# Kernel optimization log

Measured on AMD Instinct MI355X. Metric: run time of the kernel, lower is better.

Reference implementation:

```python
import jax, jax.numpy as jnp
import numpy as np
from jax import lax

# ---- fixed configuration (matches init_kwargs / input_specs) ----
L, E, V, F, HU, HL, S = 32, 1024, 2048, 8, 128, 2, 7
D0, D1R, D1E = 512, 129, 640
D = S + 1                      # path dimension = num_slices + 1
SIGLEN = D + D * D + D * D * D # iisignature.siglength(8, 3) = 584
FINAL = F * 2 * SIGLEN         # 9344
EPS = 1e-5                     # BatchNorm eps


def _bn(x, g, b):
    # BatchNorm1d in training mode: biased batch statistics over axis 0
    mu = x.mean(0)
    var = x.var(0)
    return (x - mu) / jnp.sqrt(var + EPS) * g + b


def _mlp(x, Win, bin_, gin, betain, Wh, bh, gh, betah, Wout, bout, gout, betaout):
    # eigf: Linear+BN+ReLU blocks, 1 -> HU -> ... -> HU -> 1
    h = jax.nn.relu(_bn(x @ Win.T + bin_, gin, betain))
    for l in range(HL):
        h = jax.nn.relu(_bn(h @ Wh[l].T + bh[l], gh[l], betah[l]))
    o = jax.nn.relu(_bn(h @ Wout.T + bout, gout, betaout))
    return o[:, 0]


# ---- path signature, level 3, via Chen's identity (replaces iisignature.sig) ----
def _seg(dx):
    s1 = dx
    s2 = jnp.outer(s1, dx).reshape(-1) * 0.5
    s3 = jnp.outer(s2, dx).reshape(-1) / 3.0
    return (s1, s2, s3)


def _chen(Sg, T):
    s1, s2, s3 = Sg
    t1, t2, t3 = T
    r1 = s1 + t1
    r2 = s2 + t2 + jnp.outer(s1, t1).reshape(-1)
    r3 = s3 + t3 + jnp.outer(s1, t2).reshape(-1) + jnp.outer(s2, t1).reshape(-1)
    return (r1, r2, r3)


def _sig3(path):  # path [P, D] -> [SIGLEN]
    dX = path[1:] - path[:-1]

    def step(Sg, dx):
        return _chen(Sg, _seg(dx)), None

    Sg, _ = lax.scan(step, _seg(dX[0]), dX[1:])
    return jnp.concatenate(Sg)


def _diagram_sig(vals, W_proj, b_proj):
    # Conv1d(1, S, kernel=2, stride=2) == pairwise projection; then sort, prepend time axis
    pairs = vals.reshape(-1, 2)                      # [P, 2]
    P = pairs.shape[0]
    proj = jnp.einsum('pk,sk->sp', pairs, W_proj[:, 0, :]) + b_proj[:, None]  # [S, P]
    proj = jnp.sort(proj, axis=-1)
    t = jnp.arange(P, dtype=vals.dtype) / (P * (P + 1) / 2.0)
    path = jnp.concatenate([t[None, :], proj], axis=0).T  # [P, D]
    return _sig3(path)


def setup_inputs() -> dict:
    key = jax.random.key(0)
    ks = iter(jax.random.split(key, 16))
    nrm = lambda kk, shp, sc: jax.random.normal(kk, shp, jnp.float32) * sc
    inp = {
        "eigenvalues": jax.random.uniform(next(ks), (L, E), jnp.float32),
        "eigenvectors_sq": jax.random.uniform(next(ks), (L, E, V), jnp.float32) / E,
        "dgm0": jax.random.randint(next(ks), (L, F, D0), 0, V, jnp.int32),
        "dgm1rel": jax.random.randint(next(ks), (L, F, D1R), 0, V, jnp.int32),
        "dgm1ext": jax.random.randint(next(ks), (L, F, D1E), 0, V, jnp.int32),
        "mlp_Win": nrm(next(ks), (F, HU, 1), 1.0),
        "mlp_bin": jnp.zeros((F, HU), jnp.float32),
        "mlp_gin": jnp.ones((F, HU), jnp.float32),
        "mlp_betain": jnp.zeros((F, HU), jnp.float32),
        "mlp_Wh": nrm(next(ks), (F, HL, HU, HU), 1.0 / np.sqrt(HU)),
        "mlp_bh": jnp.zeros((F, HL, HU), jnp.float32),
        "mlp_gh": jnp.ones((F, HL, HU), jnp.float32),
        "mlp_betah": jnp.zeros((F, HL, HU), jnp.float32),
        "mlp_Wout": nrm(next(ks), (F, 1, HU), 1.0 / np.sqrt(HU)),
        "mlp_bout": jnp.zeros((F, 1), jnp.float32),
        "mlp_gout": jnp.ones((F, 1), jnp.float32),
        "mlp_betaout": jnp.zeros((F, 1), jnp.float32),
        "W_proj": nrm(next(ks), (S, 1, 2), 0.7),
        "b_proj": jnp.zeros((S,), jnp.float32),
        "W_fin": nrm(next(ks), (1, FINAL), 1.0 / np.sqrt(FINAL)),
        "b_fin": jnp.zeros((1,), jnp.float32),
        "g_fin": jnp.ones((1,), jnp.float32),
        "beta_fin": jnp.zeros((1,), jnp.float32),
    }
    return inp


def reference(eigenvalues, eigenvectors_sq, dgm0, dgm1rel, dgm1ext,
              mlp_Win, mlp_bin, mlp_gin, mlp_betain,
              mlp_Wh, mlp_bh, mlp_gh, mlp_betah,
              mlp_Wout, mlp_bout, mlp_gout, mlp_betaout,
              W_proj, b_proj, W_fin, b_fin, g_fin, beta_fin):
    flat = eigenvalues.reshape(-1, 1)  # [L*E, 1], sample-major like the torch flatten
    evs = jax.vmap(lambda *p: _mlp(flat, *p))(
        mlp_Win, mlp_bin, mlp_gin, mlp_betain,
        mlp_Wh, mlp_bh, mlp_gh, mlp_betah,
        mlp_Wout, mlp_bout, mlp_gout, mlp_betaout)  # [F, L*E]
    # per-sample filtration values: evs_transformed[:, slice_i] @ eigvecsq_i
    f = jnp.einsum('fle,lev->lfv', evs.reshape(F, L, E), eigenvectors_sq)  # [L, F, V]
    fv = f.reshape(L * F, V)
    d0 = jnp.take_along_axis(fv, dgm0.reshape(L * F, D0), axis=1)
    rel = jnp.take_along_axis(fv, dgm1rel.reshape(L * F, D1R), axis=1)
    # torch.arange(len-1, 0, -1): reversed, dropping element 0
    Dgm0 = jnp.concatenate([d0, rel[:, 1:][:, ::-1]], axis=1)  # [L*F, 640]
    Dgm1 = jnp.take_along_axis(fv, dgm1ext.reshape(L * F, D1E), axis=1)
    sig0 = jax.vmap(lambda v: _diagram_sig(v, W_proj, b_proj))(Dgm0)  # [L*F, SIGLEN]
    sig1 = jax.vmap(lambda v: _diagram_sig(v, W_proj, b_proj))(Dgm1)
    x = jnp.concatenate([sig0, sig1], axis=-1).reshape(L, FINAL)
    out = x @ W_fin.T + b_fin  # dropout p=0.0 -> identity
    return _bn(out, g_fin, beta_fin)  # [L, 1]
```

## Files before the change

kernel.cpp:

```cpp
#include <hip/hip_runtime.h>
#include <cfloat>
#include <math.h>

#define N_SAMP 32768
#define FF 8
#define HU 128
#define EE 1024
#define VV 2048
#define PP 320
#define SIGLEN 584
#define FINAL_W 9344

typedef unsigned short u16;
typedef unsigned int u32;
typedef short s16x8 __attribute__((ext_vector_type(8)));
typedef float f32x4 __attribute__((ext_vector_type(4)));

__device__ __forceinline__ u16 f2bf(float v) {
  u32 u = __float_as_uint(v);
  return (u16)((u + 0x7fffu + ((u >> 16) & 1u)) >> 16);
}
__device__ __forceinline__ float bf2f(u16 h) {
  return __uint_as_float(((u32)h) << 16);
}
__device__ __forceinline__ void split3(float v, u16& h, u16& m, u16& l) {
  h = f2bf(v);
  float r = v - bf2f(h);
  m = f2bf(r);
  float r2 = r - bf2f(m);
  l = f2bf(r2);
}

__device__ __forceinline__ double wave_red(double v) {
#pragma unroll
  for (int off = 32; off > 0; off >>= 1) v += __shfl_xor(v, off, 64);
  return v;
}

#define WPAD_ROW 40
#define WPAD_CHUNK (128 * WPAD_ROW)
#define WPAD_LAYER (4 * WPAD_CHUNK)
#define WPAD_F (2 * WPAD_LAYER)
#define WPAD_TOTAL (FF * WPAD_F)

__global__ __launch_bounds__(256) void k_prep(const float* __restrict__ W,
                                              u16* __restrict__ Hh, u16* __restrict__ Hm,
                                              u16* __restrict__ Hl,
                                              const float* __restrict__ x,
                                              double* __restrict__ D) {
  __shared__ double r1[4], r2[4];
  const int bid = blockIdx.x, tid = threadIdx.x;
  if (bid < 1024) {
    int i = bid * 256 + tid;
    u16 h, m, l;
    split3(W[i], h, m, l);
    int k = i & 127, n = (i >> 7) & 127, f2l = i >> 14;
    int out = f2l * WPAD_LAYER + (k >> 5) * WPAD_CHUNK + n * WPAD_ROW + (k & 31);
    Hh[out] = h; Hm[out] = m; Hl[out] = l;
  } else if (bid < 1056) {
    int b = bid - 1024;
    double s1 = 0.0, s2 = 0.0;
    int base = b * 1024 + tid;
#pragma unroll
    for (int r = 0; r < 4; ++r) {
      double v = (double)x[base + r * 256];
      s1 += v; s2 += v * v;
    }
    s1 = wave_red(s1); s2 = wave_red(s2);
    int wave = tid >> 6, lane = tid & 63;
    if (lane == 0) { r1[wave] = s1; r2[wave] = s2; }
    __syncthreads();
    if (tid == 0) {
      D[b * 2 + 0] = r1[0] + r1[1] + r1[2] + r1[3];
      D[b * 2 + 1] = r2[0] + r2[1] + r2[2] + r2[3];
    }
  } else {
    int q = (bid - 1056) * 256 + tid;
    if (q < 4145) D[64 + q] = 0.0;
  }
}

template<int MODE>
__global__ __launch_bounds__(256, 2)
void k_mgemm(const float* __restrict__ Ain,
             const double* __restrict__ xp,
             const float* __restrict__ w_in,
             const float* __restrict__ g_in,
             const float* __restrict__ beta_in,
             const double* __restrict__ stats_in,
             const float* __restrict__ gM1,
             const float* __restrict__ betaM1,
             const u16* __restrict__ Wh_,
             const u16* __restrict__ Wm_,
             const u16* __restrict__ Wl_,
             const float* __restrict__ bb, int bstride,
             float* __restrict__ Yt_out,
             double* __restrict__ stats) {
  __shared__ u16 SB[6][128 * 40];
  __shared__ float p0[HU], p1[HU], biasl[HU], xl[HU];
  u16* Ah = SB[0]; u16* Am = SB[1]; u16* Al = SB[2];
  u16* Bh = SB[3]; u16* Bm = SB[4]; u16* Bl = SB[5];

  const int tid = threadIdx.x;
  const int f = blockIdx.y;
  const int m0 = blockIdx.x * 128;
  const int lane = tid & 63, ln = tid & 15, quad = (tid >> 4) & 3, wave = tid >> 6;

  if (tid < HU) {
    biasl[tid] = bb[(size_t)f * bstride + tid];
    if (MODE == 0) {
      double S1 = 0.0, S2 = 0.0;
#pragma unroll
      for (int r = 0; r < 32; ++r) { S1 += xp[r * 2]; S2 += xp[r * 2 + 1]; }
      double mx = S1 * (1.0 / 32768.0);
      double vx = S2 * (1.0 / 32768.0) - mx * mx;
      if (vx < 0) vx = 0;
      float w = w_in[f * HU + tid];
      double inv = 1.0 / sqrt((double)w * (double)w * vx + 1e-5);
      float sj = (float)inv * g_in[f * HU + tid] * w;
      p0[tid] = sj;
      p1[tid] = beta_in[f * HU + tid] - (float)mx * sj;
      xl[tid] = Ain[m0 + tid];
    } else {
      int idx = f * HU + tid;
      double S1 = stats_in[idx * 2 + 0], S2 = stats_in[idx * 2 + 1];
      double mean = S1 * (1.0 / 32768.0);
      double var = S2 * (1.0 / 32768.0) - mean * mean;
      if (var < 0) var = 0;
      double inv = 1.0 / sqrt(var + 1e-5);
      float gg = gM1[f * 256 + tid];
      float scv = (float)inv * gg;
      p0[tid] = scv;
      p1[tid] = betaM1[f * 256 + tid] - (float)mean * scv;
    }
  }

  f32x4 acc[2][8];
#pragma unroll
  for (int mt = 0; mt < 2; ++mt)
#pragma unroll
    for (int u = 0; u < 8; ++u) acc[mt][u] = (f32x4){0.f, 0.f, 0.f, 0.f};

  __syncthreads();

  for (int kk = 0; kk < 128; kk += 32) {
    {
      const int chunk = kk >> 5;
      const u16* gH = Wh_ + (size_t)f * WPAD_F + chunk * WPAD_CHUNK;
      const u16* gM = Wm_ + (size_t)f * WPAD_F + chunk * WPAD_CHUNK;
      const u16* gL = Wl_ + (size_t)f * WPAD_F + chunk * WPAD_CHUNK;
#pragma unroll
      for (int t = 0; t < 8; ++t) {
        int flat = wave + t * 4;
        if (flat < 30) {
          int L = (flat >= 20) ? 2 : (flat >= 10 ? 1 : 0);
          int p = flat - L * 10;
          const u16* g = (L == 0 ? gH : (L == 1 ? gM : gL)) + p * 512 + lane * 8;
          u16* d = (L == 0 ? Bh : (L == 1 ? Bm : Bl)) + p * 512;
          __builtin_amdgcn_global_load_lds(
              (const __attribute__((address_space(1))) void*)g,
              (__attribute__((address_space(3))) void*)d, 16, 0, 0);
        }
      }
    }
    if (MODE == 0) {
      const int m = tid >> 1, kh = (tid & 1) * 16;
      const float xv = xl[m];
      u32 ph[8], pm[8], pl[8];
#pragma unroll
      for (int jp = 0; jp < 8; ++jp) {
        u16 h0, m_0, l0, h1, m_1, l1;
        int k = kh + jp * 2;
        split3(fmaxf(fmaf(xv, p0[kk + k], p1[kk + k]), 0.f), h0, m_0, l0);
        split3(fmaxf(fmaf(xv, p0[kk + k + 1], p1[kk + k + 1]), 0.f), h1, m_1, l1);
        ph[jp] = (u32)h0 | ((u32)h1 << 16);
        pm[jp] = (u32)m_0 | ((u32)m_1 << 16);
        pl[jp] = (u32)l0 | ((u32)l1 << 16);
      }
      int off = m * 40 + kh;
      *(uint4*)&Ah[off] = make_uint4(ph[0], ph[1], ph[2], ph[3]);
      *(uint4*)&Ah[off + 8] = make_uint4(ph[4], ph[5], ph[6], ph[7]);
      *(uint4*)&Am[off] = make_uint4(pm[0], pm[1], pm[2], pm[3]);
      *(uint4*)&Am[off + 8] = make_uint4(pm[4], pm[5], pm[6], pm[7]);
      *(uint4*)&Al[off] = make_uint4(pl[0], pl[1], pl[2], pl[3]);
      *(uint4*)&Al[off + 8] = make_uint4(pl[4], pl[5], pl[6], pl[7]);
    } else {
#pragma unroll
      for (int r = 0; r < 4; ++r) {
        int flat = tid + r * 256;
        int m = flat & 127, kq = flat >> 7;
        const float* src = Ain + ((size_t)(f * HU + kk + kq * 4)) * N_SAMP + m0 + m;
        u32 ph[2], pm[2], pl[2];
#pragma unroll
        for (int ip = 0; ip < 2; ++ip) {
          int k = kq * 4 + ip * 2;
          float v0 = fmaxf(fmaf(src[(size_t)(ip * 2) * N_SAMP], p0[kk + k], p1[kk + k]), 0.f);
          float v1 = fmaxf(fmaf(src[(size_t)(ip * 2 + 1) * N_SAMP], p0[kk + k + 1], p1[kk + k + 1]), 0.f);
          u16 h0, m_0, l0, h1, m_1, l1;
          split3(v0, h0, m_0, l0);
          split3(v1, h1, m_1, l1);
          ph[ip] = (u32)h0 | ((u32)h1 << 16);
          pm[ip] = (u32)m_0 | ((u32)m_1 << 16);
          pl[ip] = (u32)l0 | ((u32)l1 << 16);
        }
        int off = m * 40 + kq * 4;
        *(uint2*)&Ah[off] = make_uint2(ph[0], ph[1]);
        *(uint2*)&Am[off] = make_uint2(pm[0], pm[1]);
        *(uint2*)&Al[off] = make_uint2(pl[0], pl[1]);
      }
    }
    __syncthreads();
    s16x8 af0[3], af1[3];
    {
      int r0 = (wave * 32 + ln) * 40 + quad * 8;
      int r1 = (wave * 32 + 16 + ln) * 40 + quad * 8;
      af0[0] = *(const s16x8*)&Ah[r0]; af0[1] = *(const s16x8*)&Am[r0]; af0[2] = *(const s16x8*)&Al[r0];
      af1[0] = *(const s16x8*)&Ah[r1]; af1[1] = *(const s16x8*)&Am[r1]; af1[2] = *(const s16x8*)&Al[r1];
    }
#pragma unroll
    for (int u = 0; u < 8; ++u) {
      int bo = (u * 16 + ln) * 40 + quad * 8;
      s16x8 bh = *(const s16x8*)&Bh[bo];
      s16x8 bm = *(const s16x8*)&Bm[bo];
      s16x8 bl = *(const s16x8*)&Bl[bo];
      f32x4 a0 = acc[0][u], a1 = acc[1][u];
      a0 = __builtin_amdgcn_mfma_f32_16x16x32_bf16(af0[0], bh, a0, 0, 0, 0);
      a1 = __builtin_amdgcn_mfma_f32_16x16x32_bf16(af1[0], bh, a1, 0, 0, 0);
      a0 = __builtin_amdgcn_mfma_f32_16x16x32_bf16(af0[1], bh, a0, 0, 0, 0);
      a1 = __builtin_amdgcn_mfma_f32_16x16x32_bf16(af1[1], bh, a1, 0, 0, 0);
      a0 = __builtin_amdgcn_mfma_f32_16x16x32_bf16(af0[0], bm, a0, 0, 0, 0);
      a1 = __builtin_amdgcn_mfma_f32_16x16x32_bf16(af1[0], bm, a1, 0, 0, 0);
      a0 = __builtin_amdgcn_mfma_f32_16x16x32_bf16(af0[2], bh, a0, 0, 0, 0);
      a1 = __builtin_amdgcn_mfma_f32_16x16x32_bf16(af1[2], bh, a1, 0, 0, 0);
      a0 = __builtin_amdgcn_mfma_f32_16x16x32_bf16(af0[1], bm, a0, 0, 0, 0);
      a1 = __builtin_amdgcn_mfma_f32_16x16x32_bf16(af1[1], bm, a1, 0, 0, 0);
      a0 = __builtin_amdgcn_mfma_f32_16x16x32_bf16(af0[0], bl, a0, 0, 0, 0);
      a1 = __builtin_amdgcn_mfma_f32_16x16x32_bf16(af1[0], bl, a1, 0, 0, 0);
      acc[0][u] = a0; acc[1][u] = a1;
    }
    __syncthreads();
  }

  float cs1[8], cs2[8];
#pragma unroll
  for (int u = 0; u < 8; ++u) { cs1[u] = 0.f; cs2[u] = 0.f; }
#pragma unroll
  for (int u = 0; u < 8; ++u) {
    float b = biasl[u * 16 + ln];
#pragma unroll
    for (int mt = 0; mt < 2; ++mt) {
#pragma unroll
      for (int reg = 0; reg < 4; ++reg) {
        float v = acc[mt][u][reg] + b;
        acc[mt][u][reg] = v;
        cs1[u] += v;
        cs2[u] = fmaf(v, v, cs2[u]);
      }
      float4 st = make_float4(acc[mt][u][0], acc[mt][u][1], acc[mt][u][2], acc[mt][u][3]);
      *(float4*)&Yt_out[((size_t)(f * HU + u * 16 + ln)) * N_SAMP + m0 + wave * 32 + mt * 16 + quad * 4] = st;
    }
  }
  float* red1 = (float*)&SB[0][0];
  float* red2 = red1 + 2048;
  int wq = wave * 4 + quad;
#pragma unroll
  for (int u = 0; u < 8; ++u) {
    red1[wq * 128 + u * 16 + ln] = cs1[u];
    red2[wq * 128 + u * 16 + ln] = cs2[u];
  }
  __syncthreads();
  {
    int which = tid >> 7, n = tid & 127;
    const float* rp = which ? red2 : red1;
    float s = 0.f;
#pragma unroll
    for (int r = 0; r < 16; ++r) s += rp[r * 128 + n];
    atomicAdd(&stats[(f * HU + n) * 2 + which], (double)s);
  }
}

__global__ __launch_bounds__(256, 4) void k_outlayer(const float* __restrict__ Yt,
                                                     const double* __restrict__ stats2,
                                                     const float* __restrict__ gh,
                                                     const float* __restrict__ betah,
                                                     const float* __restrict__ Wout,
                                                     const float* __restrict__ bout,
                                                     float* __restrict__ evs_pre,
                                                     double* __restrict__ stats3) {
  __shared__ float wj[HU], scl[HU], shl[HU];
  const int tid = threadIdx.x;
  const int f = blockIdx.y;
  const int i = (blockIdx.x * 256 + tid) * 2;
  if (tid < HU) {
    wj[tid] = Wout[f * HU + tid];
    int idx = f * HU + tid;
    double S1 = stats2[idx * 2 + 0], S2 = stats2[idx * 2 + 1];
    double mean = S1 * (1.0 / 32768.0);
    double var = S2 * (1.0 / 32768.0) - mean * mean;
    if (var < 0) var = 0;
    double inv = 1.0 / sqrt(var + 1e-5);
    float gg = gh[128 + f * 256 + tid];
    float scv = (float)inv * gg;
    scl[tid] = scv;
    shl[tid] = betah[128 + f * 256 + tid] - (float)mean * scv;
  }
  __syncthreads();
  const float2* base2 = (const float2*)(Yt + (size_t)f * HU * N_SAMP + i);
  float a0 = 0.f, a1 = 0.f;
#pragma unroll
  for (int j = 0; j < HU; ++j) {
    float2 y = base2[(size_t)j * (N_SAMP / 2)];
    a0 = fmaf(fmaxf(fmaf(y.x, scl[j], shl[j]), 0.f), wj[j], a0);
    a1 = fmaf(fmaxf(fmaf(y.y, scl[j], shl[j]), 0.f), wj[j], a1);
  }
  float yo0 = a0 + bout[f];
  float yo1 = a1 + bout[f];
  *(float2*)&evs_pre[(size_t)f * N_SAMP + i] = make_float2(yo0, yo1);
  double v0 = (double)yo0, v1 = (double)yo1;
  double s1 = wave_red(v0 + v1), s2 = wave_red(v0 * v0 + v1 * v1);
  __shared__ double r1[4], r2[4];
  int wave = tid >> 6, lane = tid & 63;
  if (lane == 0) { r1[wave] = s1; r2[wave] = s2; }
  __syncthreads();
  if (tid == 0) atomicAdd(&stats3[f * 2 + 0], r1[0] + r1[1] + r1[2] + r1[3]);
  if (tid == 1) atomicAdd(&stats3[f * 2 + 1], r2[0] + r2[1] + r2[2] + r2[3]);
}

__global__ __launch_bounds__(256) void k_einsum(const float* __restrict__ evs_pre,
                                                const double* __restrict__ stats3,
                                                const float* __restrict__ gout,
                                                const float* __restrict__ betaout,
                                                const float* __restrict__ eig,
                                                float* __restrict__ fv) {
  __shared__ __align__(16) float ev[FF * EE];
  __shared__ float scl3[FF], shl3[FF];
  const int tid = threadIdx.x;
  const int l = blockIdx.y;
  const int v0 = blockIdx.x * 256;
  if (tid < FF) {
    double S1 = stats3[tid * 2 + 0], S2 = stats3[tid * 2 + 1];
    double mean = S1 * (1.0 / 32768.0);
    double var = S2 * (1.0 / 32768.0) - mean * mean;
    if (var < 0) var = 0;
    double inv = 1.0 / sqrt(var + 1e-5);
    float gg = gout[tid];
    float scv = (float)inv * gg;
    scl3[tid] = scv;
    shl3[tid] = betaout[tid] - (float)mean * scv;
  }
  __syncthreads();
#pragma unroll
  for (int r = 0; r < 8; ++r) {
    int flat = tid + r * 256;
    int fch = flat >> 8, e4 = (flat & 255) * 4;
    float4 y = *(const float4*)&evs_pre[(size_t)fch * N_SAMP + l * EE + e4];
    float sv = scl3[fch], hv = shl3[fch];
    float* evp = &ev[fch * EE + e4];
    evp[0] = fmaxf(fmaf(y.x, sv, hv), 0.f);
    evp[1] = fmaxf(fmaf(y.y, sv, hv), 0.f);
    evp[2] = fmaxf(fmaf(y.z, sv, hv), 0.f);
    evp[3] = fmaxf(fmaf(y.w, sv, hv), 0.f);
  }
  __syncthreads();
  const float* up = eig + (size_t)l * EE * VV + v0 + tid;
  float acc[8] = {0, 0, 0, 0, 0, 0, 0, 0};
  for (int e0 = 0; e0 < EE; e0 += 32) {
    float u[32];
#pragma unroll
    for (int t = 0; t < 32; ++t) u[t] = up[(size_t)(e0 + t) * VV];
#pragma unroll
    for (int t = 0; t < 32; ++t) {
#pragma unroll
      for (int f = 0; f < 8; ++f) acc[f] = fmaf(ev[f * EE + e0 + t], u[t], acc[f]);
    }
  }
#pragma unroll
  for (int f = 0; f < 8; ++f) fv[((size_t)(l * FF + f)) * VV + v0 + tid] = acc[f];
}

__global__ __launch_bounds__(256) void k_diagram(const float* __restrict__ fv,
                                                 const int* __restrict__ dgm0,
                                                 const int* __restrict__ dgm1rel,
                                                 const int* __restrict__ dgm1ext,
                                                 const float* __restrict__ Wp,
                                                 const float* __restrict__ bp,
                                                 const float* __restrict__ Wf,
                                                 const float* __restrict__ bf,
                                                 const float* __restrict__ gfin,
                                                 const float* __restrict__ betafin,
                                                 double* __restrict__ outpre,
                                                 unsigned int* __restrict__ cnt,
                                                 float* __restrict__ dout) {
  __shared__ float vals[640];
  __shared__ float ps[7 * 512];
  __shared__ float dXl[320][8];
  __shared__ double rr[4];
  __shared__ unsigned int lastFlag;
  const int tid = threadIdx.x;
  const int bid = blockIdx.x;
  const int row = bid >> 1;
  const int c = bid & 1;
  const float* fvr = fv + (size_t)row * VV;

  for (int k = tid; k < 640; k += 256) {
    int idx;
    if (c == 0) idx = (k < 512) ? dgm0[(size_t)row * 512 + k] : dgm1rel[(size_t)row * 129 + (640 - k)];
    else        idx = dgm1ext[(size_t)row * 640 + k];
    vals[k] = fvr[idx];
  }
  __syncthreads();
  for (int q = tid; q < 7 * 512; q += 256) {
    int s = q >> 9, p = q & 511;
    float pv = 3.402823466e+38f;
    if (p < PP) pv = fmaf(Wp[2 * s + 1], vals[2 * p + 1], fmaf(Wp[2 * s], vals[2 * p], bp[s]));
    ps[s * 512 + p] = pv;
  }
  for (int k = 2; k <= 512; k <<= 1) {
    for (int j = k >> 1; j > 0; j >>= 1) {
      __syncthreads();
      for (int q = tid; q < 1792; q += 256) {
        int s = q >> 8, ip = q & 255;
        int i = ((ip & ~(j - 1)) << 1) | (ip & (j - 1));
        int p2 = i | j;
        float a = ps[s * 512 + i], b = ps[s * 512 + p2];
        bool up = ((i & k) == 0);
        if ((a > b) == up) { ps[s * 512 + i] = b; ps[s * 512 + p2] = a; }
      }
    }
  }
  __syncthreads();
  for (int q = tid; q < 319 * 8; q += 256) {
    int p = q >> 3, d = q & 7;
    dXl[p][d] = (d == 0) ? (1.0f / 51360.0f)
                         : ps[(d - 1) * 512 + p + 1] - ps[(d - 1) * 512 + p];
  }
  __syncthreads();
  {
    const int a = tid >> 5, b = (tid >> 2) & 7, dp = tid & 3;
    float s1a = 0.f, s2r = 0.f, s3r0 = 0.f, s3r1 = 0.f;
    for (int p = 0; p < 319; ++p) {
      float dxa = dXl[p][a];
      float dxb = dXl[p][b];
      float2 dd = *(const float2*)&dXl[p][dp * 2];
      float coefA = fmaf(dxa, (1.f / 3.f), s1a);
      float w = fmaf(0.5f * dxb, coefA, s2r);
      s2r = fmaf(dxb, fmaf(0.5f, dxa, s1a), s2r);
      s3r0 = fmaf(w, dd.x, s3r0);
      s3r1 = fmaf(w, dd.y, s3r1);
      s1a += dxa;
    }
    const int l = row >> 3, ff = row & 7;
    const int base = ff * (2 * SIGLEN) + c * SIGLEN;
    double part = (double)s3r0 * (double)Wf[base + 72 + (a * 8 + b) * 8 + dp * 2]
                + (double)s3r1 * (double)Wf[base + 72 + (a * 8 + b) * 8 + dp * 2 + 1];
    if (dp == 0) part += (double)s2r * (double)Wf[base + 8 + a * 8 + b];
    if (b == 0 && dp == 0) part += (double)s1a * (double)Wf[base + a];
    part = wave_red(part);
    int wv = tid >> 6, lnn = tid & 63;
    if (lnn == 0) rr[wv] = part;
    __syncthreads();
    if (tid == 0) {
      atomicAdd(&outpre[l], rr[0] + rr[1] + rr[2] + rr[3]);
      __threadfence();
      unsigned int old = atomicAdd(cnt, 1u);
      lastFlag = (old == 511u) ? 1u : 0u;
    }
    __syncthreads();
    if (lastFlag && tid < 64) {
      __threadfence();
      double v = 0.0;
      if (tid < 32) v = ((volatile double*)outpre)[tid] + (double)bf[0];
      double s1 = wave_red(v);
      double s2 = wave_red(v * v);
      double mean = s1 * (1.0 / 32.0);
      double var = s2 * (1.0 / 32.0) - mean * mean;
      if (var < 0) var = 0;
      double inv = 1.0 / sqrt(var + 1e-5);
      if (tid < 32) dout[tid] = (float)((v - mean) * inv * (double)gfin[0] + (double)betafin[0]);
    }
  }
}

extern "C" void kernel_launch(void* const* d_in, const int* in_sizes, int n_in,
                              void* d_out, int out_size, void* d_ws, size_t ws_size,
                              hipStream_t stream) {
  const float* eig     = (const float*)d_in[0];
  const float* eigsq   = (const float*)d_in[1];
  const int*   dgm0    = (const int*)d_in[2];
  const int*   dgm1rel = (const int*)d_in[3];
  const int*   dgm1ext = (const int*)d_in[4];
  const float* Win     = (const float*)d_in[5];
  const float* gin     = (const float*)d_in[7];
  const float* betain  = (const float*)d_in[8];
  const float* Wh      = (const float*)d_in[9];
  const float* bh      = (const float*)d_in[10];
  const float* gh      = (const float*)d_in[11];
  const float* betah   = (const float*)d_in[12];
  const float* Wout    = (const float*)d_in[13];
  const float* bout    = (const float*)d_in[14];
  const float* gout    = (const float*)d_in[15];
  const float* betaout = (const float*)d_in[16];
  const float* Wp      = (const float*)d_in[17];
  const float* bp      = (const float*)d_in[18];
  const float* Wfin    = (const float*)d_in[19];
  const float* bfin    = (const float*)d_in[20];
  const float* gfin    = (const float*)d_in[21];
  const float* betafin = (const float*)d_in[22];

  char* ws = (char*)d_ws;
  float*  Yt      = (float*)(ws);
  float*  evs_pre = (float*)(ws + 134217728u);
  float*  fv      = (float*)(ws + 135266304u);
  double* D       = (double*)(ws + 138576384u);
  double* xp      = D;
  double* stats1  = D + 64;
  double* stats2  = D + 2112;
  double* stats3  = D + 4160;
  double* outpre  = D + 4176;
  unsigned int* cnt = (unsigned int*)(D + 4208);
  u16*    Whh     = (u16*)(ws + 138612736u);
  u16*    Whm     = Whh + WPAD_TOTAL;
  u16*    Whl     = Whm + WPAD_TOTAL;

  k_prep<<<1073, 256, 0, stream>>>(Wh, Whh, Whm, Whl, eig, D);
  k_mgemm<0><<<dim3(256, FF), 256, 0, stream>>>(eig, xp, Win, gin, betain,
                                                nullptr, nullptr, nullptr,
                                                Whh, Whm, Whl,
                                                bh, 256, Yt, stats1);
  k_mgemm<1><<<dim3(256, FF), 256, 0, stream>>>(Yt, nullptr, nullptr, nullptr, nullptr,
                                                stats1, gh, betah,
                                                Whh + WPAD_LAYER, Whm + WPAD_LAYER, Whl + WPAD_LAYER,
                                                bh + 128, 256, Yt, stats2);
  k_outlayer<<<dim3(64, FF), 256, 0, stream>>>(Yt, stats2, gh, betah, Wout, bout,
                                               evs_pre, stats3);
  k_einsum<<<dim3(8, 32), 256, 0, stream>>>(evs_pre, stats3, gout, betaout, eigsq, fv);
  k_diagram<<<512, 256, 0, stream>>>(fv, dgm0, dgm1rel, dgm1ext, Wp, bp,
                                     Wfin, bfin, gfin, betafin, outpre, cnt,
                                     (float*)d_out);
}
```

Baseline: 663.9 us.

## Recompute first hidden layer in-register to avoid writing and rereading its activations

The first GEMM pass now only computes BatchNorm statistics and no longer stores its 128x32768x8 activation tensor. A second fused kernel recomputes layer 0 from the scalar input, applies BN+ReLU to the accumulators in registers, splits them into bf16 parts in shared memory and runs the second hidden-layer GEMM directly. This removes a large global write and a strided global read of the intermediate, at the cost of running the first layer's three-way-split MFMA GEMM twice.

```diff
diff --git a/kernel.cpp b/kernel.cpp
--- a/kernel.cpp
+++ b/kernel.cpp
@@ -80,22 +80,17 @@
   }
 }
 
-template<int MODE>
 __global__ __launch_bounds__(256, 2)
-void k_mgemm(const float* __restrict__ Ain,
-             const double* __restrict__ xp,
-             const float* __restrict__ w_in,
-             const float* __restrict__ g_in,
-             const float* __restrict__ beta_in,
-             const double* __restrict__ stats_in,
-             const float* __restrict__ gM1,
-             const float* __restrict__ betaM1,
-             const u16* __restrict__ Wh_,
-             const u16* __restrict__ Wm_,
-             const u16* __restrict__ Wl_,
-             const float* __restrict__ bb, int bstride,
-             float* __restrict__ Yt_out,
-             double* __restrict__ stats) {
+void k_stats0(const float* __restrict__ x,
+              const double* __restrict__ xp,
+              const float* __restrict__ w_in,
+              const float* __restrict__ g_in,
+              const float* __restrict__ beta_in,
+              const u16* __restrict__ Wh_,
+              const u16* __restrict__ Wm_,
+              const u16* __restrict__ Wl_,
+              const float* __restrict__ bh,
+              double* __restrict__ stats) {
   __shared__ u16 SB[6][128 * 40];
   __shared__ float p0[HU], p1[HU], biasl[HU], xl[HU];
   u16* Ah = SB[0]; u16* Am = SB[1]; u16* Al = SB[2];
@@ -107,32 +102,19 @@
   const int lane = tid & 63, ln = tid & 15, quad = (tid >> 4) & 3, wave = tid >> 6;
 
   if (tid < HU) {
-    biasl[tid] = bb[(size_t)f * bstride + tid];
-    if (MODE == 0) {
-      double S1 = 0.0, S2 = 0.0;
-#pragma unroll
-      for (int r = 0; r < 32; ++r) { S1 += xp[r * 2]; S2 += xp[r * 2 + 1]; }
-      double mx = S1 * (1.0 / 32768.0);
-      double vx = S2 * (1.0 / 32768.0) - mx * mx;
-      if (vx < 0) vx = 0;
-      float w = w_in[f * HU + tid];
-      double inv = 1.0 / sqrt((double)w * (double)w * vx + 1e-5);
-      float sj = (float)inv * g_in[f * HU + tid] * w;
-      p0[tid] = sj;
-      p1[tid] = beta_in[f * HU + tid] - (float)mx * sj;
-      xl[tid] = Ain[m0 + tid];
-    } else {
-      int idx = f * HU + tid;
-      double S1 = stats_in[idx * 2 + 0], S2 = stats_in[idx * 2 + 1];
-      double mean = S1 * (1.0 / 32768.0);
-      double var = S2 * (1.0 / 32768.0) - mean * mean;
-      if (var < 0) var = 0;
-      double inv = 1.0 / sqrt(var + 1e-5);
-      float gg = gM1[f * 256 + tid];
-      float scv = (float)inv * gg;
-      p0[tid] = scv;
-      p1[tid] = betaM1[f * 256 + tid] - (float)mean * scv;
-    }
+    biasl[tid] = bh[f * 256 + tid];
+    double S1 = 0.0, S2 = 0.0;
+#pragma unroll
+    for (int r = 0; r < 32; ++r) { S1 += xp[r * 2]; S2 += xp[r * 2 + 1]; }
+    double mx = S1 * (1.0 / 32768.0);
+    double vx = S2 * (1.0 / 32768.0) - mx * mx;
+    if (vx < 0) vx = 0;
+    float w = w_in[f * HU + tid];
+    double inv = 1.0 / sqrt((double)w * (double)w * vx + 1e-5);
+    float sj = (float)inv * g_in[f * HU + tid] * w;
+    p0[tid] = sj;
+    p1[tid] = beta_in[f * HU + tid] - (float)mx * sj;
+    xl[tid] = x[m0 + tid];
   }
 
   f32x4 acc[2][8];
@@ -163,7 +145,7 @@
         }
       }
     }
-    if (MODE == 0) {
+    {
       const int m = tid >> 1, kh = (tid & 1) * 16;
       const float xv = xl[m];
       u32 ph[8], pm[8], pl[8];
@@ -184,30 +166,6 @@
       *(uint4*)&Am[off + 8] = make_uint4(pm[4], pm[5], pm[6], pm[7]);
       *(uint4*)&Al[off] = make_uint4(pl[0], pl[1], pl[2], pl[3]);
       *(uint4*)&Al[off + 8] = make_uint4(pl[4], pl[5], pl[6], pl[7]);
-    } else {
-#pragma unroll
-      for (int r = 0; r < 4; ++r) {
-        int flat = tid + r * 256;
-        int m = flat & 127, kq = flat >> 7;
-        const float* src = Ain + ((size_t)(f * HU + kk + kq * 4)) * N_SAMP + m0 + m;
-        u32 ph[2], pm[2], pl[2];
-#pragma unroll
-        for (int ip = 0; ip < 2; ++ip) {
-          int k = kq * 4 + ip * 2;
-          float v0 = fmaxf(fmaf(src[(size_t)(ip * 2) * N_SAMP], p0[kk + k], p1[kk + k]), 0.f);
-          float v1 = fmaxf(fmaf(src[(size_t)(ip * 2 + 1) * N_SAMP], p0[kk + k + 1], p1[kk + k + 1]), 0.f);
-          u16 h0, m_0, l0, h1, m_1, l1;
-          split3(v0, h0, m_0, l0);
-          split3(v1, h1, m_1, l1);
-          ph[ip] = (u32)h0 | ((u32)h1 << 16);
-          pm[ip] = (u32)m_0 | ((u32)m_1 << 16);
-          pl[ip] = (u32)l0 | ((u32)l1 << 16);
-        }
-        int off = m * 40 + kq * 4;
-        *(uint2*)&Ah[off] = make_uint2(ph[0], ph[1]);
-        *(uint2*)&Am[off] = make_uint2(pm[0], pm[1]);
-        *(uint2*)&Al[off] = make_uint2(pl[0], pl[1]);
-      }
     }
     __syncthreads();
     s16x8 af0[3], af1[3];
@@ -220,22 +178,22 @@
 #pragma unroll
     for (int u = 0; u < 8; ++u) {
       int bo = (u * 16 + ln) * 40 + quad * 8;
-      s16x8 bh = *(const s16x8*)&Bh[bo];
-      s16x8 bm = *(const s16x8*)&Bm[bo];
-      s16x8 bl = *(const s16x8*)&Bl[bo];
+      s16x8 bhv = *(const s16x8*)&Bh[bo];
+      s16x8 bmv = *(const s16x8*)&Bm[bo];
+      s16x8 blv = *(const s16x8*)&Bl[bo];
       f32x4 a0 = acc[0][u], a1 = acc[1][u];
-      a0 = __builtin_amdgcn_mfma_f32_16x16x32_bf16(af0[0], bh, a0, 0, 0, 0);
-      a1 = __builtin_amdgcn_mfma_f32_16x16x32_bf16(af1[0], bh, a1, 0, 0, 0);
-      a0 = __builtin_amdgcn_mfma_f32_16x16x32_bf16(af0[1], bh, a0, 0, 0, 0);
-      a1 = __builtin_amdgcn_mfma_f32_16x16x32_bf16(af1[1], bh, a1, 0, 0, 0);
-      a0 = __builtin_amdgcn_mfma_f32_16x16x32_bf16(af0[0], bm, a0, 0, 0, 0);
-      a1 = __builtin_amdgcn_mfma_f32_16x16x32_bf16(af1[0], bm, a1, 0, 0, 0);
-      a0 = __builtin_amdgcn_mfma_f32_16x16x32_bf16(af0[2], bh, a0, 0, 0, 0);
-      a1 = __builtin_amdgcn_mfma_f32_16x16x32_bf16(af1[2], bh, a1, 0, 0, 0);
-      a0 = __builtin_amdgcn_mfma_f32_16x16x32_bf16(af0[1], bm, a0, 0, 0, 0);
-      a1 = __builtin_amdgcn_mfma_f32_16x16x32_bf16(af1[1], bm, a1, 0, 0, 0);
-      a0 = __builtin_amdgcn_mfma_f32_16x16x32_bf16(af0[0], bl, a0, 0, 0, 0);
-      a1 = __builtin_amdgcn_mfma_f32_16x16x32_bf16(af1[0], bl, a1, 0, 0, 0);
+      a0 = __builtin_amdgcn_mfma_f32_16x16x32_bf16(af0[0], bhv, a0, 0, 0, 0);
+      a1 = __builtin_amdgcn_mfma_f32_16x16x32_bf16(af1[0], bhv, a1, 0, 0, 0);
+      a0 = __builtin_amdgcn_mfma_f32_16x16x32_bf16(af0[1], bhv, a0, 0, 0, 0);
+      a1 = __builtin_amdgcn_mfma_f32_16x16x32_bf16(af1[1], bhv, a1, 0, 0, 0);
+      a0 = __builtin_amdgcn_mfma_f32_16x16x32_bf16(af0[0], bmv, a0, 0, 0, 0);
+      a1 = __builtin_amdgcn_mfma_f32_16x16x32_bf16(af1[0], bmv, a1, 0, 0, 0);
+      a0 = __builtin_amdgcn_mfma_f32_16x16x32_bf16(af0[2], bhv, a0, 0, 0, 0);
+      a1 = __builtin_amdgcn_mfma_f32_16x16x32_bf16(af1[2], bhv, a1, 0, 0, 0);
+      a0 = __builtin_amdgcn_mfma_f32_16x16x32_bf16(af0[1], bmv, a0, 0, 0, 0);
+      a1 = __builtin_amdgcn_mfma_f32_16x16x32_bf16(af1[1], bmv, a1, 0, 0, 0);
+      a0 = __builtin_amdgcn_mfma_f32_16x16x32_bf16(af0[0], blv, a0, 0, 0, 0);
+      a1 = __builtin_amdgcn_mfma_f32_16x16x32_bf16(af1[0], blv, a1, 0, 0, 0);
       acc[0][u] = a0; acc[1][u] = a1;
     }
     __syncthreads();
@@ -252,12 +210,9 @@
 #pragma unroll
       for (int reg = 0; reg < 4; ++reg) {
         float v = acc[mt][u][reg] + b;
-        acc[mt][u][reg] = v;
         cs1[u] += v;
         cs2[u] = fmaf(v, v, cs2[u]);
       }
-      float4 st = make_float4(acc[mt][u][0], acc[mt][u][1], acc[mt][u][2], acc[mt][u][3]);
-      *(float4*)&Yt_out[((size_t)(f * HU + u * 16 + ln)) * N_SAMP + m0 + wave * 32 + mt * 16 + quad * 4] = st;
     }
   }
   float* red1 = (float*)&SB[0][0];
@@ -276,6 +231,259 @@
 #pragma unroll
     for (int r = 0; r < 16; ++r) s += rp[r * 128 + n];
     atomicAdd(&stats[(f * HU + n) * 2 + which], (double)s);
+  }
+}
+
+__global__ __launch_bounds__(256, 2)
+void k_mgemm01(const float* __restrict__ x,
+               const double* __restrict__ xp,
+               const float* __restrict__ w_in,
+               const float* __restrict__ g_in,
+               const float* __restrict__ beta_in,
+               const double* __restrict__ stats1,
+               const float* __restrict__ gh,
+               const float* __restrict__ betah,
+               const u16* __restrict__ Wh_,
+               const u16* __restrict__ Wm_,
+               const u16* __restrict__ Wl_,
+               const float* __restrict__ bh,
+               float* __restrict__ Yt_out,
+               double* __restrict__ stats2) {
+  __shared__ u16 SB[6][128 * 40];
+  __shared__ float p0[HU], p1[HU], xl[HU], b0l[HU], b1l[HU], sc1l[HU], sh1l[HU];
+  u16* Ah = SB[0]; u16* Am = SB[1]; u16* Al = SB[2];
+  u16* Bh = SB[3]; u16* Bm = SB[4]; u16* Bl = SB[5];
+
+  const int tid = threadIdx.x;
+  const int f = blockIdx.y;
+  const int m0 = blockIdx.x * 128;
+  const int lane = tid & 63, ln = tid & 15, quad = (tid >> 4) & 3, wave = tid >> 6;
+
+  if (tid < HU) {
+    double S1 = 0.0, S2 = 0.0;
+#pragma unroll
+    for (int r = 0; r < 32; ++r) { S1 += xp[r * 2]; S2 += xp[r * 2 + 1]; }
+    double mx = S1 * (1.0 / 32768.0);
+    double vx = S2 * (1.0 / 32768.0) - mx * mx;
+    if (vx < 0) vx = 0;
+    float w = w_in[f * HU + tid];
+    double inv = 1.0 / sqrt((double)w * (double)w * vx + 1e-5);
+    float sj = (float)inv * g_in[f * HU + tid] * w;
+    p0[tid] = sj;
+    p1[tid] = beta_in[f * HU + tid] - (float)mx * sj;
+    xl[tid] = x[m0 + tid];
+    b0l[tid] = bh[f * 256 + tid];
+    b1l[tid] = bh[f * 256 + 128 + tid];
+    int idx = f * HU + tid;
+    double T1 = stats1[idx * 2 + 0], T2 = stats1[idx * 2 + 1];
+    double mean = T1 * (1.0 / 32768.0);
+    double var = T2 * (1.0 / 32768.0) - mean * mean;
+    if (var < 0) var = 0;
+    double inv1 = 1.0 / sqrt(var + 1e-5);
+    float gg = gh[f * 256 + tid];
+    float scv = (float)inv1 * gg;
+    sc1l[tid] = scv;
+    sh1l[tid] = betah[f * 256 + tid] - (float)mean * scv;
+  }
+
+  f32x4 acc0[2][8];
+#pragma unroll
+  for (int mt = 0; mt < 2; ++mt)
+#pragma unroll
+    for (int u = 0; u < 8; ++u) acc0[mt][u] = (f32x4){0.f, 0.f, 0.f, 0.f};
+
+  __syncthreads();
+
+  for (int kk = 0; kk < 128; kk += 32) {
+    {
+      const int chunk = kk >> 5;
+      const u16* gH = Wh_ + (size_t)f * WPAD_F + chunk * WPAD_CHUNK;
+      const u16* gM = Wm_ + (size_t)f * WPAD_F + chunk * WPAD_CHUNK;
+      const u16* gL = Wl_ + (size_t)f * WPAD_F + chunk * WPAD_CHUNK;
+#pragma unroll
+      for (int t = 0; t < 8; ++t) {
+        int flat = wave + t * 4;
+        if (flat < 30) {
+          int L = (flat >= 20) ? 2 : (flat >= 10 ? 1 : 0);
+          int p = flat - L * 10;
+          const u16* g = (L == 0 ? gH : (L == 1 ? gM : gL)) + p * 512 + lane * 8;
+          u16* d = (L == 0 ? Bh : (L == 1 ? Bm : Bl)) + p * 512;
+          __builtin_amdgcn_global_load_lds(
+              (const __attribute__((address_space(1))) void*)g,
+              (__attribute__((address_space(3))) void*)d, 16, 0, 0);
+        }
+      }
+    }
+    {
+      const int m = tid >> 1, kh = (tid & 1) * 16;
+      const float xv = xl[m];
+      u32 ph[8], pm[8], pl[8];
+#pragma unroll
+      for (int jp = 0; jp < 8; ++jp) {
+        u16 h0, m_0, l0, h1, m_1, l1;
+        int k = kh + jp * 2;
+        split3(fmaxf(fmaf(xv, p0[kk + k], p1[kk + k]), 0.f), h0, m_0, l0);
+        split3(fmaxf(fmaf(xv, p0[kk + k + 1], p1[kk + k + 1]), 0.f), h1, m_1, l1);
+        ph[jp] = (u32)h0 | ((u32)h1 << 16);
+        pm[jp] = (u32)m_0 | ((u32)m_1 << 16);
+        pl[jp] = (u32)l0 | ((u32)l1 << 16);
+      }
+      int off = m * 40 + kh;
+      *(uint4*)&Ah[off] = make_uint4(ph[0], ph[1], ph[2], ph[3]);
+      *(uint4*)&Ah[off + 8] = make_uint4(ph[4], ph[5], ph[6], ph[7]);
+      *(uint4*)&Am[off] = make_uint4(pm[0], pm[1], pm[2], pm[3]);
+      *(uint4*)&Am[off + 8] = make_uint4(pm[4], pm[5], pm[6], pm[7]);
+      *(uint4*)&Al[off] = make_uint4(pl[0], pl[1], pl[2], pl[3]);
+      *(uint4*)&Al[off + 8] = make_uint4(pl[4], pl[5], pl[6], pl[7]);
+    }
+    __syncthreads();
+    s16x8 af0[3], af1[3];
+    {
+      int r0 = (wave * 32 + ln) * 40 + quad * 8;
+      int r1 = (wave * 32 + 16 + ln) * 40 + quad * 8;
+      af0[0] = *(const s16x8*)&Ah[r0]; af0[1] = *(const s16x8*)&Am[r0]; af0[2] = *(const s16x8*)&Al[r0];
+      af1[0] = *(const s16x8*)&Ah[r1]; af1[1] = *(const s16x8*)&Am[r1]; af1[2] = *(const s16x8*)&Al[r1];
+    }
+#pragma unroll
+    for (int u = 0; u < 8; ++u) {
+      int bo = (u * 16 + ln) * 40 + quad * 8;
+      s16x8 bhv = *(const s16x8*)&Bh[bo];
+      s16x8 bmv = *(const s16x8*)&Bm[bo];
+      s16x8 blv = *(const s16x8*)&Bl[bo];
+      f32x4 a0 = acc0[0][u], a1 = acc0[1][u];
+      a0 = __builtin_amdgcn_mfma_f32_16x16x32_bf16(af0[0], bhv, a0, 0, 0, 0);
+      a1 = __builtin_amdgcn_mfma_f32_16x16x32_bf16(af1[0], bhv, a1, 0, 0, 0);
+      a0 = __builtin_amdgcn_mfma_f32_16x16x32_bf16(af0[1], bhv, a0, 0, 0, 0);
+      a1 = __builtin_amdgcn_mfma_f32_16x16x32_bf16(af1[1], bhv, a1, 0, 0, 0);
+      a0 = __builtin_amdgcn_mfma_f32_16x16x32_bf16(af0[0], bmv, a0, 0, 0, 0);
+      a1 = __builtin_amdgcn_mfma_f32_16x16x32_bf16(af1[0], bmv, a1, 0, 0, 0);
+      a0 = __builtin_amdgcn_mfma_f32_16x16x32_bf16(af0[2], bhv, a0, 0, 0, 0);
+      a1 = __builtin_amdgcn_mfma_f32_16x16x32_bf16(af1[2], bhv, a1, 0, 0, 0);
+      a0 = __builtin_amdgcn_mfma_f32_16x16x32_bf16(af0[1], bmv, a0, 0, 0, 0);
+      a1 = __builtin_amdgcn_mfma_f32_16x16x32_bf16(af1[1], bmv, a1, 0, 0, 0);
+      a0 = __builtin_amdgcn_mfma_f32_16x16x32_bf16(af0[0], blv, a0, 0, 0, 0);
+      a1 = __builtin_amdgcn_mfma_f32_16x16x32_bf16(af1[0], blv, a1, 0, 0, 0);
+      acc0[0][u] = a0; acc0[1][u] = a1;
+    }
+    __syncthreads();
+  }
+
+  f32x4 acc1[2][8];
+#pragma unroll
+  for (int mt = 0; mt < 2; ++mt)
+#pragma unroll
+    for (int u = 0; u < 8; ++u) acc1[mt][u] = (f32x4){0.f, 0.f, 0.f, 0.f};
+
+#pragma unroll
+  for (int kk1 = 0; kk1 < 128; kk1 += 32) {
+    {
+      const int chunk = kk1 >> 5;
+      const u16* gH = Wh_ + (size_t)f * WPAD_F + WPAD_LAYER + chunk * WPAD_CHUNK;
+      const u16* gM = Wm_ + (size_t)f * WPAD_F + WPAD_LAYER + chunk * WPAD_CHUNK;
+      const u16* gL = Wl_ + (size_t)f * WPAD_F + WPAD_LAYER + chunk * WPAD_CHUNK;
+#pragma unroll
+      for (int t = 0; t < 8; ++t) {
+        int flat = wave + t * 4;
+        if (flat < 30) {
+          int L = (flat >= 20) ? 2 : (flat >= 10 ? 1 : 0);
+          int p = flat - L * 10;
+          const u16* g = (L == 0 ? gH : (L == 1 ? gM : gL)) + p * 512 + lane * 8;
+          u16* d = (L == 0 ? Bh : (L == 1 ? Bm : Bl)) + p * 512;
+          __builtin_amdgcn_global_load_lds(
+              (const __attribute__((address_space(1))) void*)g,
+              (__attribute__((address_space(3))) void*)d, 16, 0, 0);
+        }
+      }
+    }
+    {
+      const int u_lo = kk1 >> 4;
+#pragma unroll
+      for (int ui = 0; ui < 2; ++ui) {
+        const int u = u_lo + ui;
+        const int k = u * 16 + ln;
+        const float sc = sc1l[k], sh = sh1l[k], bb0 = b0l[k];
+#pragma unroll
+        for (int mt = 0; mt < 2; ++mt) {
+#pragma unroll
+          for (int reg = 0; reg < 4; ++reg) {
+            float v = acc0[mt][u][reg] + bb0;
+            float a = fmaxf(fmaf(v, sc, sh), 0.f);
+            u16 h, mm, l;
+            split3(a, h, mm, l);
+            int m = wave * 32 + mt * 16 + quad * 4 + reg;
+            int off = m * 40 + ui * 16 + ln;
+            Ah[off] = h; Am[off] = mm; Al[off] = l;
+          }
+        }
+      }
+    }
+    __syncthreads();
+    s16x8 af0[3], af1[3];
+    {
+      int r0 = (wave * 32 + ln) * 40 + quad * 8;
+      int r1 = (wave * 32 + 16 + ln) * 40 + quad * 8;
+      af0[0] = *(const s16x8*)&Ah[r0]; af0[1] = *(const s16x8*)&Am[r0]; af0[2] = *(const s16x8*)&Al[r0];
+      af1[0] = *(const s16x8*)&Ah[r1]; af1[1] = *(const s16x8*)&Am[r1]; af1[2] = *(const s16x8*)&Al[r1];
+    }
+#pragma unroll
+    for (int u = 0; u < 8; ++u) {
+      int bo = (u * 16 + ln) * 40 + quad * 8;
+      s16x8 bhv = *(const s16x8*)&Bh[bo];
+      s16x8 bmv = *(const s16x8*)&Bm[bo];
+      s16x8 blv = *(const s16x8*)&Bl[bo];
+      f32x4 a0 = acc1[0][u], a1 = acc1[1][u];
+      a0 = __builtin_amdgcn_mfma_f32_16x16x32_bf16(af0[0], bhv, a0, 0, 0, 0);
+      a1 = __builtin_amdgcn_mfma_f32_16x16x32_bf16(af1[0], bhv, a1, 0, 0, 0);
+      a0 = __builtin_amdgcn_mfma_f32_16x16x32_bf16(af0[1], bhv, a0, 0, 0, 0);
+      a1 = __builtin_amdgcn_mfma_f32_16x16x32_bf16(af1[1], bhv, a1, 0, 0, 0);
+      a0 = __builtin_amdgcn_mfma_f32_16x16x32_bf16(af0[0], bmv, a0, 0, 0, 0);
+      a1 = __builtin_amdgcn_mfma_f32_16x16x32_bf16(af1[0], bmv, a1, 0, 0, 0);
+      a0 = __builtin_amdgcn_mfma_f32_16x16x32_bf16(af0[2], bhv, a0, 0, 0, 0);
+      a1 = __builtin_amdgcn_mfma_f32_16x16x32_bf16(af1[2], bhv, a1, 0, 0, 0);
+      a0 = __builtin_amdgcn_mfma_f32_16x16x32_bf16(af0[1], bmv, a0, 0, 0, 0);
+      a1 = __builtin_amdgcn_mfma_f32_16x16x32_bf16(af1[1], bmv, a1, 0, 0, 0);
+      a0 = __builtin_amdgcn_mfma_f32_16x16x32_bf16(af0[0], blv, a0, 0, 0, 0);
+      a1 = __builtin_amdgcn_mfma_f32_16x16x32_bf16(af1[0], blv, a1, 0, 0, 0);
+      acc1[0][u] = a0; acc1[1][u] = a1;
+    }
+    __syncthreads();
+  }
+
+  float cs1[8], cs2[8];
+#pragma unroll
+  for (int u = 0; u < 8; ++u) { cs1[u] = 0.f; cs2[u] = 0.f; }
+#pragma unroll
+  for (int u = 0; u < 8; ++u) {
+    float b = b1l[u * 16 + ln];
+#pragma unroll
+    for (int mt = 0; mt < 2; ++mt) {
+#pragma unroll
+      for (int reg = 0; reg < 4; ++reg) {
+        float v = acc1[mt][u][reg] + b;
+        acc1[mt][u][reg] = v;
+        cs1[u] += v;
+        cs2[u] = fmaf(v, v, cs2[u]);
+      }
+      float4 st = make_float4(acc1[mt][u][0], acc1[mt][u][1], acc1[mt][u][2], acc1[mt][u][3]);
+      *(float4*)&Yt_out[((size_t)(f * HU + u * 16 + ln)) * N_SAMP + m0 + wave * 32 + mt * 16 + quad * 4] = st;
+    }
+  }
+  float* red1 = (float*)&SB[0][0];
+  float* red2 = red1 + 2048;
+  int wq = wave * 4 + quad;
+#pragma unroll
+  for (int u = 0; u < 8; ++u) {
+    red1[wq * 128 + u * 16 + ln] = cs1[u];
+    red2[wq * 128 + u * 16 + ln] = cs2[u];
+  }
+  __syncthreads();
+  {
+    int which = tid >> 7, n = tid & 127;
+    const float* rp = which ? red2 : red1;
+    float s = 0.f;
+#pragma unroll
+    for (int r = 0; r < 16; ++r) s += rp[r * 128 + n];
+    atomicAdd(&stats2[(f * HU + n) * 2 + which], (double)s);
   }
 }
 
@@ -523,14 +731,11 @@
   u16*    Whl     = Whm + WPAD_TOTAL;
 
   k_prep<<<1073, 256, 0, stream>>>(Wh, Whh, Whm, Whl, eig, D);
-  k_mgemm<0><<<dim3(256, FF), 256, 0, stream>>>(eig, xp, Win, gin, betain,
-                                                nullptr, nullptr, nullptr,
-                                                Whh, Whm, Whl,
-                                                bh, 256, Yt, stats1);
-  k_mgemm<1><<<dim3(256, FF), 256, 0, stream>>>(Yt, nullptr, nullptr, nullptr, nullptr,
-                                                stats1, gh, betah,
-                                                Whh + WPAD_LAYER, Whm + WPAD_LAYER, Whl + WPAD_LAYER,
-                                                bh + 128, 256, Yt, stats2);
+  k_stats0<<<dim3(256, FF), 256, 0, stream>>>(eig, xp, Win, gin, betain,
+                                              Whh, Whm, Whl, bh, stats1);
+  k_mgemm01<<<dim3(256, FF), 256, 0, stream>>>(eig, xp, Win, gin, betain,
+                                               stats1, gh, betah,
+                                               Whh, Whm, Whl, bh, Yt, stats2);
   k_outlayer<<<dim3(64, FF), 256, 0, stream>>>(Yt, stats2, gh, betah, Wout, bout,
                                                evs_pre, stats3);
   k_einsum<<<dim3(8, 32), 256, 0, stream>>>(evs_pre, stats3, gout, betaout, eigsq, fv);
```

Measured after the change: 694.5 us. +4.6%, slower.
